# Optimization experiments

Measured on AMD Instinct MI355X. Metric: run time of the kernel, lower is better.

The kernel has to match this reference:

```python
import jax, jax.numpy as jnp
import numpy as np

B, S, H = 4, 2048, 768
NH, DH = 12, 64
WH = 128
EPS = 1e-12


def layer_norm(x, w, b, eps=EPS):
    mu = jnp.mean(x, axis=-1, keepdims=True)
    var = jnp.var(x, axis=-1, keepdims=True)
    return (x - mu) * jax.lax.rsqrt(var + eps) * w + b


def setup_inputs() -> dict:
    key = jax.random.key(0)
    ks = jax.random.split(key, 12)
    std = 0.02
    inp = {
        "hidden_states": jax.random.normal(ks[0], (B, S, H), jnp.float32),
        "attention_mask": jnp.ones((B, S), jnp.float32),
        "Wq": jax.random.normal(ks[1], (H, H), jnp.float32) * std,
        "bq": jnp.zeros((H,), jnp.float32),
        "Wk": jax.random.normal(ks[2], (H, H), jnp.float32) * std,
        "bk": jnp.zeros((H,), jnp.float32),
        "Wv": jax.random.normal(ks[3], (H, H), jnp.float32) * std,
        "bv": jnp.zeros((H,), jnp.float32),
        "Wg1": jax.random.normal(ks[4], (H, WH), jnp.float32) * std,
        "bg1": jnp.zeros((WH,), jnp.float32),
        "g_ln_w": jnp.ones((WH,), jnp.float32),
        "g_ln_b": jnp.zeros((WH,), jnp.float32),
        "Wg2": jax.random.normal(ks[5], (WH, NH), jnp.float32) * std,
        "bg2": jnp.zeros((NH,), jnp.float32),
        "Wo": jax.random.normal(ks[6], (H, H), jnp.float32) * std,
        "bo": jnp.zeros((H,), jnp.float32),
        "ln_w": jnp.ones((H,), jnp.float32),
        "ln_b": jnp.zeros((H,), jnp.float32),
    }
    return inp


def reference(hidden_states, attention_mask, Wq, bq, Wk, bk, Wv, bv,
              Wg1, bg1, g_ln_w, g_ln_b, Wg2, bg2, Wo, bo, ln_w, ln_b):
    b, s, _ = hidden_states.shape

    def heads(x):  # [b,s,H] -> [b,nh,s,dh]
        return x.reshape(b, s, NH, DH).transpose(0, 2, 1, 3)

    q = heads(hidden_states @ Wq + bq)
    k = heads(hidden_states @ Wk + bk)
    v = heads(hidden_states @ Wv + bv)

    scores = jnp.einsum("bhqd,bhkd->bhqk", q, k) / jnp.sqrt(jnp.float32(DH))

    # wormhole gate: per (batch, query-position, head) sigmoid scalar
    g = hidden_states @ Wg1 + bg1
    g = layer_norm(g, g_ln_w, g_ln_b)
    g = jax.nn.relu(g) @ Wg2 + bg2
    gates = jax.nn.sigmoid(g)                       # [b,s,nh]
    gates = gates.transpose(0, 2, 1)[..., None]     # [b,nh,s,1]
    scores = scores * gates

    mask = (1.0 - attention_mask) * -10000.0        # [b,s]
    scores = scores + mask[:, None, None, :]        # broadcast over heads/query

    probs = jax.nn.softmax(scores, axis=-1)         # dropout is identity in eval
    ctx = jnp.einsum("bhqk,bhkd->bhqd", probs, v)
    ctx = ctx.transpose(0, 2, 1, 3).reshape(b, s, H)

    out = ctx @ Wo + bo
    out = layer_norm(out + hidden_states, ln_w, ln_b)
    return out, probs
```

## Files before the change

kernel.cpp:

```cpp
#include <hip/hip_runtime.h>
#include <math.h>

#define Bn  4
#define Sn  2048
#define Hn  768
#define NHn 12
#define DHn 64
#define WHn 128
#define MR  (Bn * Sn)
#define EPSf 1e-12f

__global__ __launch_bounds__(256) void proj_gemm(const float* __restrict__ A,
                                                 const float* __restrict__ W,
                                                 const float* __restrict__ bias,
                                                 float* __restrict__ C,
                                                 int M, int N, int K) {
    __shared__ float At[16][68];
    __shared__ float Bs[16][68];
    const int tid = threadIdx.x;
    const int tx = tid & 15, ty = tid >> 4;
    const int row0 = blockIdx.y << 6, col0 = blockIdx.x << 6;
    float acc[4][4] = {};

    for (int k0 = 0; k0 < K; k0 += 16) {
        {
            const int r = tid >> 2;
            const int c = (tid & 3) << 2;
            float4 av = *(const float4*)(A + (size_t)(row0 + r) * K + (k0 + c));
            At[c + 0][r] = av.x; At[c + 1][r] = av.y;
            At[c + 2][r] = av.z; At[c + 3][r] = av.w;
            const int wr = tid >> 4;
            const int wc = (tid & 15) << 2;
            *(float4*)&Bs[wr][wc] =
                *(const float4*)(W + (size_t)(k0 + wr) * N + (col0 + wc));
        }
        __syncthreads();
#pragma unroll
        for (int kk = 0; kk < 16; ++kk) {
            float4 a4 = *(const float4*)&At[kk][ty << 2];
            float4 b4 = *(const float4*)&Bs[kk][tx << 2];
            const float a[4] = {a4.x, a4.y, a4.z, a4.w};
            const float b[4] = {b4.x, b4.y, b4.z, b4.w};
#pragma unroll
            for (int i = 0; i < 4; ++i)
#pragma unroll
                for (int j = 0; j < 4; ++j) acc[i][j] += a[i] * b[j];
        }
        __syncthreads();
    }
#pragma unroll
    for (int i = 0; i < 4; ++i) {
        const int r = row0 + (ty << 2) + i;
        const int c = col0 + (tx << 2);
        float4 o;
        o.x = acc[i][0] + bias[c + 0];
        o.y = acc[i][1] + bias[c + 1];
        o.z = acc[i][2] + bias[c + 2];
        o.w = acc[i][3] + bias[c + 3];
        *(float4*)(C + (size_t)r * N + c) = o;
    }
}

__global__ __launch_bounds__(128) void gate_kernel(const float* __restrict__ g,
                                                   const float* __restrict__ lw,
                                                   const float* __restrict__ lb,
                                                   const float* __restrict__ Wg2,
                                                   const float* __restrict__ bg2,
                                                   float* __restrict__ gates) {
    const int row = blockIdx.x;
    const int t = threadIdx.x;
    __shared__ float red[128];
    __shared__ float ys[128];
    const float x = g[(size_t)row * WHn + t];
    red[t] = x; __syncthreads();
    for (int s2 = 64; s2 > 0; s2 >>= 1) {
        if (t < s2) red[t] += red[t + s2];
        __syncthreads();
    }
    const float mu = red[0] * (1.0f / WHn);
    __syncthreads();
    const float d = x - mu;
    red[t] = d * d; __syncthreads();
    for (int s2 = 64; s2 > 0; s2 >>= 1) {
        if (t < s2) red[t] += red[t + s2];
        __syncthreads();
    }
    const float var = red[0] * (1.0f / WHn);
    float y = d * rsqrtf(var + EPSf) * lw[t] + lb[t];
    y = fmaxf(y, 0.0f);
    ys[t] = y; __syncthreads();
    if (t < NHn) {
        float acc = bg2[t];
        for (int w = 0; w < WHn; ++w) acc += ys[w] * Wg2[w * NHn + t];
        gates[(size_t)row * NHn + t] = 1.0f / (1.0f + __expf(-acc));
    }
}

__global__ __launch_bounds__(256) void scores_kernel(const float* __restrict__ qb,
                                                     const float* __restrict__ kb,
                                                     const float* __restrict__ gates,
                                                     const float* __restrict__ amask,
                                                     float* __restrict__ probs) {
    __shared__ float Qt[64][68];
    __shared__ float Kt[64][68];
    const int tid = threadIdx.x;
    const int tx = tid & 15, ty = tid >> 4;
    const int bh = blockIdx.z;
    const int b = bh / NHn, h = bh - b * NHn;
    const int q0 = blockIdx.y << 6, c0 = blockIdx.x << 6;
    const float* Q  = qb + (size_t)b * Sn * Hn + (size_t)h * DHn;
    const float* Kp = kb + (size_t)b * Sn * Hn + (size_t)h * DHn;

#pragma unroll
    for (int t2 = 0; t2 < 4; ++t2) {
        const int f = tid + (t2 << 8);
        const int r = f >> 4;
        const int c = (f & 15) << 2;
        float4 qv = *(const float4*)(Q + (size_t)(q0 + r) * Hn + c);
        Qt[c + 0][r] = qv.x; Qt[c + 1][r] = qv.y;
        Qt[c + 2][r] = qv.z; Qt[c + 3][r] = qv.w;
        float4 kv = *(const float4*)(Kp + (size_t)(c0 + r) * Hn + c);
        Kt[c + 0][r] = kv.x; Kt[c + 1][r] = kv.y;
        Kt[c + 2][r] = kv.z; Kt[c + 3][r] = kv.w;
    }
    __syncthreads();

    float acc[4][4] = {};
#pragma unroll 8
    for (int d = 0; d < 64; ++d) {
        float4 a4 = *(const float4*)&Qt[d][ty << 2];
        float4 b4 = *(const float4*)&Kt[d][tx << 2];
        const float a[4] = {a4.x, a4.y, a4.z, a4.w};
        const float b[4] = {b4.x, b4.y, b4.z, b4.w};
#pragma unroll
        for (int i = 0; i < 4; ++i)
#pragma unroll
            for (int j = 0; j < 4; ++j) acc[i][j] += a[i] * b[j];
    }

    const int cc = c0 + (tx << 2);
    float m[4];
#pragma unroll
    for (int j = 0; j < 4; ++j)
        m[j] = (1.0f - amask[(size_t)b * Sn + cc + j]) * -10000.0f;
#pragma unroll
    for (int i = 0; i < 4; ++i) {
        const int qr = q0 + (ty << 2) + i;
        const float gt = gates[((size_t)b * Sn + qr) * NHn + h] * 0.125f;
        float4 o;
        o.x = acc[i][0] * gt + m[0];
        o.y = acc[i][1] * gt + m[1];
        o.z = acc[i][2] * gt + m[2];
        o.w = acc[i][3] * gt + m[3];
        *(float4*)(probs + (size_t)bh * Sn * Sn + (size_t)qr * Sn + cc) = o;
    }
}

__global__ __launch_bounds__(256) void softmax_kernel(float* __restrict__ probs) {
    const size_t row = blockIdx.x;
    float* p = probs + row * (size_t)Sn;
    const int t = threadIdx.x;
    float4 x0 = *(float4*)(p + (t << 2));
    float4 x1 = *(float4*)(p + 1024 + (t << 2));
    float m = fmaxf(fmaxf(fmaxf(x0.x, x0.y), fmaxf(x0.z, x0.w)),
                    fmaxf(fmaxf(x1.x, x1.y), fmaxf(x1.z, x1.w)));
    __shared__ float red[256];
    red[t] = m; __syncthreads();
    for (int s2 = 128; s2 > 0; s2 >>= 1) {
        if (t < s2) red[t] = fmaxf(red[t], red[t + s2]);
        __syncthreads();
    }
    m = red[0]; __syncthreads();
    x0.x = __expf(x0.x - m); x0.y = __expf(x0.y - m);
    x0.z = __expf(x0.z - m); x0.w = __expf(x0.w - m);
    x1.x = __expf(x1.x - m); x1.y = __expf(x1.y - m);
    x1.z = __expf(x1.z - m); x1.w = __expf(x1.w - m);
    red[t] = x0.x + x0.y + x0.z + x0.w + x1.x + x1.y + x1.z + x1.w;
    __syncthreads();
    for (int s2 = 128; s2 > 0; s2 >>= 1) {
        if (t < s2) red[t] += red[t + s2];
        __syncthreads();
    }
    const float inv = 1.0f / red[0];
    x0.x *= inv; x0.y *= inv; x0.z *= inv; x0.w *= inv;
    x1.x *= inv; x1.y *= inv; x1.z *= inv; x1.w *= inv;
    *(float4*)(p + (t << 2)) = x0;
    *(float4*)(p + 1024 + (t << 2)) = x1;
}

__global__ __launch_bounds__(256) void pv_gemm(const float* __restrict__ probs,
                                               const float* __restrict__ vb,
                                               float* __restrict__ ctx) {
    __shared__ float Pt[16][68];
    __shared__ float Vs[16][68];
    const int tid = threadIdx.x;
    const int tx = tid & 15, ty = tid >> 4;
    const int bh = blockIdx.z;
    const int b = bh / NHn, h = bh - b * NHn;
    const int q0 = blockIdx.y << 6;
    const float* P = probs + (size_t)bh * Sn * Sn;
    const float* V = vb + (size_t)b * Sn * Hn + (size_t)h * DHn;
    float acc[4][4] = {};

    for (int k0 = 0; k0 < Sn; k0 += 16) {
        {
            const int r = tid >> 2;
            const int c = (tid & 3) << 2;
            float4 pv = *(const float4*)(P + (size_t)(q0 + r) * Sn + (k0 + c));
            Pt[c + 0][r] = pv.x; Pt[c + 1][r] = pv.y;
            Pt[c + 2][r] = pv.z; Pt[c + 3][r] = pv.w;
            const int wr = tid >> 4;
            const int wc = (tid & 15) << 2;
            *(float4*)&Vs[wr][wc] =
                *(const float4*)(V + (size_t)(k0 + wr) * Hn + wc);
        }
        __syncthreads();
#pragma unroll
        for (int kk = 0; kk < 16; ++kk) {
            float4 a4 = *(const float4*)&Pt[kk][ty << 2];
            float4 b4 = *(const float4*)&Vs[kk][tx << 2];
            const float a[4] = {a4.x, a4.y, a4.z, a4.w};
            const float b[4] = {b4.x, b4.y, b4.z, b4.w};
#pragma unroll
            for (int i = 0; i < 4; ++i)
#pragma unroll
                for (int j = 0; j < 4; ++j) acc[i][j] += a[i] * b[j];
        }
        __syncthreads();
    }
#pragma unroll
    for (int i = 0; i < 4; ++i) {
        const int qr = q0 + (ty << 2) + i;
        float4 o;
        o.x = acc[i][0]; o.y = acc[i][1]; o.z = acc[i][2]; o.w = acc[i][3];
        *(float4*)(ctx + ((size_t)b * Sn + qr) * Hn + h * DHn + (tx << 2)) = o;
    }
}

__global__ __launch_bounds__(256) void final_ln(const float* __restrict__ xo,
                                                const float* __restrict__ hs,
                                                const float* __restrict__ lw,
                                                const float* __restrict__ lb,
                                                float* __restrict__ out) {
    const int row = blockIdx.x;
    const int t = threadIdx.x;
    const float* a = xo + (size_t)row * Hn;
    const float* r = hs + (size_t)row * Hn;
    const float x0 = a[t] + r[t];
    const float x1 = a[t + 256] + r[t + 256];
    const float x2 = a[t + 512] + r[t + 512];
    __shared__ float red[256];
    red[t] = x0 + x1 + x2; __syncthreads();
    for (int s2 = 128; s2 > 0; s2 >>= 1) {
        if (t < s2) red[t] += red[t + s2];
        __syncthreads();
    }
    const float mu = red[0] * (1.0f / Hn);
    __syncthreads();
    const float d0 = x0 - mu, d1 = x1 - mu, d2 = x2 - mu;
    red[t] = d0 * d0 + d1 * d1 + d2 * d2; __syncthreads();
    for (int s2 = 128; s2 > 0; s2 >>= 1) {
        if (t < s2) red[t] += red[t + s2];
        __syncthreads();
    }
    const float rs = rsqrtf(red[0] * (1.0f / Hn) + EPSf);
    out[(size_t)row * Hn + t]       = d0 * rs * lw[t]       + lb[t];
    out[(size_t)row * Hn + t + 256] = d1 * rs * lw[t + 256] + lb[t + 256];
    out[(size_t)row * Hn + t + 512] = d2 * rs * lw[t + 512] + lb[t + 512];
}

extern "C" void kernel_launch(void* const* d_in, const int* in_sizes, int n_in,
                              void* d_out, int out_size, void* d_ws, size_t ws_size,
                              hipStream_t stream) {
    const float* hidden = (const float*)d_in[0];
    const float* amask  = (const float*)d_in[1];
    const float* Wq = (const float*)d_in[2];  const float* bq = (const float*)d_in[3];
    const float* Wk = (const float*)d_in[4];  const float* bk = (const float*)d_in[5];
    const float* Wv = (const float*)d_in[6];  const float* bv = (const float*)d_in[7];
    const float* Wg1 = (const float*)d_in[8]; const float* bg1 = (const float*)d_in[9];
    const float* glw = (const float*)d_in[10]; const float* glb = (const float*)d_in[11];
    const float* Wg2 = (const float*)d_in[12]; const float* bg2 = (const float*)d_in[13];
    const float* Wo = (const float*)d_in[14]; const float* bo = (const float*)d_in[15];
    const float* lw = (const float*)d_in[16]; const float* lb = (const float*)d_in[17];

    float* out   = (float*)d_out;
    float* probs = out + (size_t)MR * Hn;

    float* q     = (float*)d_ws;
    float* k     = q + (size_t)MR * Hn;
    float* v     = k + (size_t)MR * Hn;
    float* g     = v + (size_t)MR * Hn;
    float* gates = g + (size_t)MR * WHn;
    float* ctx   = k;
    float* ctxo  = q;

    dim3 blk(256);
    proj_gemm<<<dim3(Hn / 64, MR / 64), blk, 0, stream>>>(hidden, Wq, bq, q, MR, Hn, Hn);
    proj_gemm<<<dim3(Hn / 64, MR / 64), blk, 0, stream>>>(hidden, Wk, bk, k, MR, Hn, Hn);
    proj_gemm<<<dim3(Hn / 64, MR / 64), blk, 0, stream>>>(hidden, Wv, bv, v, MR, Hn, Hn);
    proj_gemm<<<dim3(WHn / 64, MR / 64), blk, 0, stream>>>(hidden, Wg1, bg1, g, MR, WHn, Hn);
    gate_kernel<<<dim3(MR), dim3(128), 0, stream>>>(g, glw, glb, Wg2, bg2, gates);
    scores_kernel<<<dim3(Sn / 64, Sn / 64, Bn * NHn), blk, 0, stream>>>(q, k, gates, amask, probs);
    softmax_kernel<<<dim3(Bn * NHn * Sn), blk, 0, stream>>>(probs);
    pv_gemm<<<dim3(1, Sn / 64, Bn * NHn), blk, 0, stream>>>(probs, v, ctx);
    proj_gemm<<<dim3(Hn / 64, MR / 64), blk, 0, stream>>>(ctx, Wo, bo, ctxo, MR, Hn, Hn);
    final_ln<<<dim3(MR), blk, 0, stream>>>(ctxo, hidden, lw, lb, out);
}
```

Measured before the change: 2.305 ms.

## Fuse scores, softmax and PV into one attention kernel with online max/sum

Replaces the separate scores, softmax and PV kernels with one kernel per (query tile, batch-head). A first pass computes the gated, masked scores, writes them raw to the probs buffer and tracks the running row max and sum with wave shuffles. A second pass rereads each score tile, normalises and writes it back as probabilities, and accumulates P·V from shared memory. This drops one full read-write pass of the probs tensor and two launches. In exchange the grid is much smaller (only Sn/64 × B·NH blocks), so occupancy may suffer, and ctx is now staged in the output buffer.

```diff
diff --git a/kernel.cpp b/kernel.cpp
--- a/kernel.cpp
+++ b/kernel.cpp
@@ -96,20 +96,24 @@
     }
 }
 
-__global__ __launch_bounds__(256) void scores_kernel(const float* __restrict__ qb,
-                                                     const float* __restrict__ kb,
-                                                     const float* __restrict__ gates,
-                                                     const float* __restrict__ amask,
-                                                     float* __restrict__ probs) {
-    __shared__ float Qt[64][68];
-    __shared__ float Kt[64][68];
+__global__ __launch_bounds__(256) void attn_fused(const float* __restrict__ qb,
+                                                  const float* __restrict__ kb,
+                                                  const float* __restrict__ vb,
+                                                  const float* __restrict__ gates,
+                                                  const float* __restrict__ amask,
+                                                  float* __restrict__ probs,
+                                                  float* __restrict__ ctx) {
+    __shared__ float SA[64][68];
+    __shared__ float SB[64][68];
     const int tid = threadIdx.x;
     const int tx = tid & 15, ty = tid >> 4;
-    const int bh = blockIdx.z;
+    const int bh = blockIdx.y;
     const int b = bh / NHn, h = bh - b * NHn;
-    const int q0 = blockIdx.y << 6, c0 = blockIdx.x << 6;
-    const float* Q  = qb + (size_t)b * Sn * Hn + (size_t)h * DHn;
-    const float* Kp = kb + (size_t)b * Sn * Hn + (size_t)h * DHn;
+    const int q0 = blockIdx.x << 6;
+    const float* Q = qb + (size_t)b * Sn * Hn + (size_t)h * DHn;
+    const float* K = kb + (size_t)b * Sn * Hn + (size_t)h * DHn;
+    const float* V = vb + (size_t)b * Sn * Hn + (size_t)h * DHn;
+    float* P = probs + (size_t)bh * Sn * Sn;
 
 #pragma unroll
     for (int t2 = 0; t2 < 4; ++t2) {
@@ -117,122 +121,135 @@
         const int r = f >> 4;
         const int c = (f & 15) << 2;
         float4 qv = *(const float4*)(Q + (size_t)(q0 + r) * Hn + c);
-        Qt[c + 0][r] = qv.x; Qt[c + 1][r] = qv.y;
-        Qt[c + 2][r] = qv.z; Qt[c + 3][r] = qv.w;
-        float4 kv = *(const float4*)(Kp + (size_t)(c0 + r) * Hn + c);
-        Kt[c + 0][r] = kv.x; Kt[c + 1][r] = kv.y;
-        Kt[c + 2][r] = kv.z; Kt[c + 3][r] = kv.w;
-    }
-    __syncthreads();
-
-    float acc[4][4] = {};
+        SA[c + 0][r] = qv.x; SA[c + 1][r] = qv.y;
+        SA[c + 2][r] = qv.z; SA[c + 3][r] = qv.w;
+    }
+
+    float gt[4];
+#pragma unroll
+    for (int i = 0; i < 4; ++i)
+        gt[i] = gates[((size_t)b * Sn + q0 + (ty << 2) + i) * NHn + h] * 0.125f;
+
+    float mrow[4] = {-INFINITY, -INFINITY, -INFINITY, -INFINITY};
+    float lrow[4] = {0.f, 0.f, 0.f, 0.f};
+
+    for (int kt = 0; kt < 32; ++kt) {
+        const int c0 = kt << 6;
+        __syncthreads();
+#pragma unroll
+        for (int t2 = 0; t2 < 4; ++t2) {
+            const int f = tid + (t2 << 8);
+            const int r = f >> 4;
+            const int c = (f & 15) << 2;
+            float4 kv = *(const float4*)(K + (size_t)(c0 + r) * Hn + c);
+            SB[c + 0][r] = kv.x; SB[c + 1][r] = kv.y;
+            SB[c + 2][r] = kv.z; SB[c + 3][r] = kv.w;
+        }
+        __syncthreads();
+
+        float acc[4][4] = {};
 #pragma unroll 8
-    for (int d = 0; d < 64; ++d) {
-        float4 a4 = *(const float4*)&Qt[d][ty << 2];
-        float4 b4 = *(const float4*)&Kt[d][tx << 2];
-        const float a[4] = {a4.x, a4.y, a4.z, a4.w};
-        const float b[4] = {b4.x, b4.y, b4.z, b4.w};
-#pragma unroll
-        for (int i = 0; i < 4; ++i)
-#pragma unroll
-            for (int j = 0; j < 4; ++j) acc[i][j] += a[i] * b[j];
-    }
-
-    const int cc = c0 + (tx << 2);
-    float m[4];
-#pragma unroll
-    for (int j = 0; j < 4; ++j)
-        m[j] = (1.0f - amask[(size_t)b * Sn + cc + j]) * -10000.0f;
-#pragma unroll
-    for (int i = 0; i < 4; ++i) {
-        const int qr = q0 + (ty << 2) + i;
-        const float gt = gates[((size_t)b * Sn + qr) * NHn + h] * 0.125f;
-        float4 o;
-        o.x = acc[i][0] * gt + m[0];
-        o.y = acc[i][1] * gt + m[1];
-        o.z = acc[i][2] * gt + m[2];
-        o.w = acc[i][3] * gt + m[3];
-        *(float4*)(probs + (size_t)bh * Sn * Sn + (size_t)qr * Sn + cc) = o;
-    }
-}
-
-__global__ __launch_bounds__(256) void softmax_kernel(float* __restrict__ probs) {
-    const size_t row = blockIdx.x;
-    float* p = probs + row * (size_t)Sn;
-    const int t = threadIdx.x;
-    float4 x0 = *(float4*)(p + (t << 2));
-    float4 x1 = *(float4*)(p + 1024 + (t << 2));
-    float m = fmaxf(fmaxf(fmaxf(x0.x, x0.y), fmaxf(x0.z, x0.w)),
-                    fmaxf(fmaxf(x1.x, x1.y), fmaxf(x1.z, x1.w)));
-    __shared__ float red[256];
-    red[t] = m; __syncthreads();
-    for (int s2 = 128; s2 > 0; s2 >>= 1) {
-        if (t < s2) red[t] = fmaxf(red[t], red[t + s2]);
-        __syncthreads();
-    }
-    m = red[0]; __syncthreads();
-    x0.x = __expf(x0.x - m); x0.y = __expf(x0.y - m);
-    x0.z = __expf(x0.z - m); x0.w = __expf(x0.w - m);
-    x1.x = __expf(x1.x - m); x1.y = __expf(x1.y - m);
-    x1.z = __expf(x1.z - m); x1.w = __expf(x1.w - m);
-    red[t] = x0.x + x0.y + x0.z + x0.w + x1.x + x1.y + x1.z + x1.w;
-    __syncthreads();
-    for (int s2 = 128; s2 > 0; s2 >>= 1) {
-        if (t < s2) red[t] += red[t + s2];
-        __syncthreads();
-    }
-    const float inv = 1.0f / red[0];
-    x0.x *= inv; x0.y *= inv; x0.z *= inv; x0.w *= inv;
-    x1.x *= inv; x1.y *= inv; x1.z *= inv; x1.w *= inv;
-    *(float4*)(p + (t << 2)) = x0;
-    *(float4*)(p + 1024 + (t << 2)) = x1;
-}
-
-__global__ __launch_bounds__(256) void pv_gemm(const float* __restrict__ probs,
-                                               const float* __restrict__ vb,
-                                               float* __restrict__ ctx) {
-    __shared__ float Pt[16][68];
-    __shared__ float Vs[16][68];
-    const int tid = threadIdx.x;
-    const int tx = tid & 15, ty = tid >> 4;
-    const int bh = blockIdx.z;
-    const int b = bh / NHn, h = bh - b * NHn;
-    const int q0 = blockIdx.y << 6;
-    const float* P = probs + (size_t)bh * Sn * Sn;
-    const float* V = vb + (size_t)b * Sn * Hn + (size_t)h * DHn;
-    float acc[4][4] = {};
-
-    for (int k0 = 0; k0 < Sn; k0 += 16) {
-        {
-            const int r = tid >> 2;
-            const int c = (tid & 3) << 2;
-            float4 pv = *(const float4*)(P + (size_t)(q0 + r) * Sn + (k0 + c));
-            Pt[c + 0][r] = pv.x; Pt[c + 1][r] = pv.y;
-            Pt[c + 2][r] = pv.z; Pt[c + 3][r] = pv.w;
-            const int wr = tid >> 4;
-            const int wc = (tid & 15) << 2;
-            *(float4*)&Vs[wr][wc] =
-                *(const float4*)(V + (size_t)(k0 + wr) * Hn + wc);
-        }
-        __syncthreads();
-#pragma unroll
-        for (int kk = 0; kk < 16; ++kk) {
-            float4 a4 = *(const float4*)&Pt[kk][ty << 2];
-            float4 b4 = *(const float4*)&Vs[kk][tx << 2];
+        for (int d = 0; d < 64; ++d) {
+            float4 a4 = *(const float4*)&SA[d][ty << 2];
+            float4 b4 = *(const float4*)&SB[d][tx << 2];
             const float a[4] = {a4.x, a4.y, a4.z, a4.w};
-            const float b[4] = {b4.x, b4.y, b4.z, b4.w};
+            const float bb[4] = {b4.x, b4.y, b4.z, b4.w};
 #pragma unroll
             for (int i = 0; i < 4; ++i)
 #pragma unroll
-                for (int j = 0; j < 4; ++j) acc[i][j] += a[i] * b[j];
-        }
-        __syncthreads();
-    }
+                for (int j = 0; j < 4; ++j) acc[i][j] += a[i] * bb[j];
+        }
+
+        const int cc = c0 + (tx << 2);
+        float mk[4];
+#pragma unroll
+        for (int j = 0; j < 4; ++j)
+            mk[j] = (1.0f - amask[(size_t)b * Sn + cc + j]) * -10000.0f;
+
+#pragma unroll
+        for (int i = 0; i < 4; ++i) {
+            const float s0 = acc[i][0] * gt[i] + mk[0];
+            const float s1 = acc[i][1] * gt[i] + mk[1];
+            const float s2 = acc[i][2] * gt[i] + mk[2];
+            const float s3 = acc[i][3] * gt[i] + mk[3];
+            const int qr = q0 + (ty << 2) + i;
+            float4 o = {s0, s1, s2, s3};
+            *(float4*)(P + (size_t)qr * Sn + cc) = o;
+
+            float tmax = fmaxf(fmaxf(s0, s1), fmaxf(s2, s3));
+#pragma unroll
+            for (int w = 1; w < 16; w <<= 1)
+                tmax = fmaxf(tmax, __shfl_xor(tmax, w, 16));
+            const float nm = fmaxf(mrow[i], tmax);
+            float ps = __expf(s0 - nm) + __expf(s1 - nm)
+                     + __expf(s2 - nm) + __expf(s3 - nm);
+#pragma unroll
+            for (int w = 1; w < 16; w <<= 1)
+                ps += __shfl_xor(ps, w, 16);
+            lrow[i] = lrow[i] * __expf(mrow[i] - nm) + ps;
+            mrow[i] = nm;
+        }
+    }
+
+    float inv[4];
+#pragma unroll
+    for (int i = 0; i < 4; ++i) inv[i] = 1.0f / lrow[i];
+
+    float cacc[4][4] = {};
+    for (int kt = 31; kt >= 0; --kt) {
+        const int c0 = kt << 6;
+        __syncthreads();
+#pragma unroll
+        for (int t2 = 0; t2 < 4; ++t2) {
+            const int f = tid + (t2 << 8);
+            const int r = f >> 4;
+            const int c = (f & 15) << 2;
+            *(float4*)&SB[r][c] = *(const float4*)(V + (size_t)(c0 + r) * Hn + c);
+        }
+        const int cc = c0 + (tx << 2);
+#pragma unroll
+        for (int i = 0; i < 4; ++i) {
+            const int qr = q0 + (ty << 2) + i;
+            float4 s = *(const float4*)(P + (size_t)qr * Sn + cc);
+            float4 p;
+            p.x = __expf(s.x - mrow[i]) * inv[i];
+            p.y = __expf(s.y - mrow[i]) * inv[i];
+            p.z = __expf(s.z - mrow[i]) * inv[i];
+            p.w = __expf(s.w - mrow[i]) * inv[i];
+            *(float4*)(P + (size_t)qr * Sn + cc) = p;
+            *(float4*)&SA[(ty << 2) + i][tx << 2] = p;
+        }
+        __syncthreads();
+#pragma unroll 4
+        for (int kk = 0; kk < 64; kk += 4) {
+            float4 a_[4], b_[4];
+#pragma unroll
+            for (int i = 0; i < 4; ++i)
+                a_[i] = *(const float4*)&SA[(ty << 2) + i][kk];
+#pragma unroll
+            for (int t2 = 0; t2 < 4; ++t2)
+                b_[t2] = *(const float4*)&SB[kk + t2][tx << 2];
+#pragma unroll
+            for (int i = 0; i < 4; ++i) {
+                const float a0 = a_[i].x, a1 = a_[i].y, a2 = a_[i].z, a3 = a_[i].w;
+#pragma unroll
+                for (int j = 0; j < 4; ++j) {
+                    const float* bj0 = &b_[0].x;
+                    cacc[i][j] += a0 * (&b_[0].x)[j];
+                    cacc[i][j] += a1 * (&b_[1].x)[j];
+                    cacc[i][j] += a2 * (&b_[2].x)[j];
+                    cacc[i][j] += a3 * (&b_[3].x)[j];
+                    (void)bj0;
+                }
+            }
+        }
+    }
+
 #pragma unroll
     for (int i = 0; i < 4; ++i) {
         const int qr = q0 + (ty << 2) + i;
         float4 o;
-        o.x = acc[i][0]; o.y = acc[i][1]; o.z = acc[i][2]; o.w = acc[i][3];
+        o.x = cacc[i][0]; o.y = cacc[i][1]; o.z = cacc[i][2]; o.w = cacc[i][3];
         *(float4*)(ctx + ((size_t)b * Sn + qr) * Hn + h * DHn + (tx << 2)) = o;
     }
 }
@@ -291,7 +308,7 @@
     float* v     = k + (size_t)MR * Hn;
     float* g     = v + (size_t)MR * Hn;
     float* gates = g + (size_t)MR * WHn;
-    float* ctx   = k;
+    float* ctx   = out;
     float* ctxo  = q;
 
     dim3 blk(256);
@@ -300,9 +317,7 @@
     proj_gemm<<<dim3(Hn / 64, MR / 64), blk, 0, stream>>>(hidden, Wv, bv, v, MR, Hn, Hn);
     proj_gemm<<<dim3(WHn / 64, MR / 64), blk, 0, stream>>>(hidden, Wg1, bg1, g, MR, WHn, Hn);
     gate_kernel<<<dim3(MR), dim3(128), 0, stream>>>(g, glw, glb, Wg2, bg2, gates);
-    scores_kernel<<<dim3(Sn / 64, Sn / 64, Bn * NHn), blk, 0, stream>>>(q, k, gates, amask, probs);
-    softmax_kernel<<<dim3(Bn * NHn * Sn), blk, 0, stream>>>(probs);
-    pv_gemm<<<dim3(1, Sn / 64, Bn * NHn), blk, 0, stream>>>(probs, v, ctx);
+    attn_fused<<<dim3(Sn / 64, Bn * NHn), blk, 0, stream>>>(q, k, v, gates, amask, probs, ctx);
     proj_gemm<<<dim3(Hn / 64, MR / 64), blk, 0, stream>>>(ctx, Wo, bo, ctxo, MR, Hn, Hn);
     final_ln<<<dim3(MR), blk, 0, stream>>>(ctxo, hidden, lw, lb, out);
 }
```

Result: faster. 2.186 ms (-5.2%).
